# Kernel optimization log

Measured on AMD Instinct MI355X. Metric: run time of the kernel, lower is better.

Reference implementation:

```python
import jax, jax.numpy as jnp
import numpy as np

BS, SEQ, H = 64, 512, 768
E, T, K = 32, 64, 64


def setup_inputs() -> dict:
    key = jax.random.key(0)
    ks = jax.random.split(key, 16)
    return {
        "hidden_states": jax.random.normal(ks[0], (BS, SEQ, H), dtype=jnp.float32),
        "Wsrc": jax.random.normal(ks[1], (862, 384), dtype=jnp.float32) * 0.02,
        "Wtgt": jax.random.normal(ks[2], (862, 384), dtype=jnp.float32) * 0.02,
        "W_cls": jax.random.normal(ks[3], (2, 6144), dtype=jnp.float32) * 0.02,
        "b_cls": jnp.zeros((2,), dtype=jnp.float32),
        "W_topic": jax.random.normal(ks[4], (2, 6144), dtype=jnp.float32) * 0.02,
        "b_topic": jnp.zeros((2,), dtype=jnp.float32),
        "W_token": jax.random.normal(ks[5], (2, 6144), dtype=jnp.float32) * 0.02,
        "b_token": jnp.zeros((2,), dtype=jnp.float32),
        "source_ids": jax.random.randint(ks[6], (BS,), 0, 862),
        "target_ids": jax.random.randint(ks[7], (BS,), 0, 862),
        "ent_inds": jax.random.randint(ks[8], (BS, E), 0, SEQ - 1),
        "ent_mask": jnp.ones((BS, E), dtype=jnp.float32),
        "topic_inds": jax.random.randint(ks[9], (BS, T), 0, SEQ),
        "topic_mask": jnp.ones((BS, T), dtype=jnp.float32),
        "token_inds": jax.random.randint(ks[10], (BS, K), 0, SEQ),
        "token_mask": jnp.ones((BS, K), dtype=jnp.float32),
    }


def reference(hidden_states, Wsrc, Wtgt, W_cls, b_cls, W_topic, b_topic,
              W_token, b_token, source_ids, target_ids, ent_inds, ent_mask,
              topic_inds, topic_mask, token_inds, token_mask):
    bs = hidden_states.shape[0]
    # domain embedding: concat(source_emb, target_emb) -> [bs, 768] -> [bs, 96, 8]
    domain = jnp.concatenate([Wsrc[source_ids], Wtgt[target_ids]], axis=1)
    d0 = domain.reshape(bs, 96, 8)

    def gather(inds, mask, offset=0):
        # ragged gather of hidden states at token positions, zero-padded slots masked
        h = jnp.take_along_axis(hidden_states, (inds + offset)[:, :, None], axis=1)
        return h * mask[:, :, None]  # [bs, L, 768]

    ent_h = gather(ent_inds, ent_mask, offset=1)
    topic_h = gather(topic_inds, topic_mask)
    token_h = gather(token_inds, token_mask)

    # CLS bilinear: outer product over the 8-dim factor, [bs,96,8,8] -> [bs,6144]
    cls_h = hidden_states[:, 0, :].reshape(bs, 96, 8)
    bl_cls = (d0[:, :, :, None] * cls_h[:, :, None, :]).reshape(bs, 6144)
    cls_logits = jax.nn.softmax(bl_cls @ W_cls.T + b_cls, axis=1)

    def bilin(h, W, b):
        h4 = h.reshape(bs, -1, 96, 8)  # [bs, L, 96, 8]
        bl = (d0[:, None, :, :, None] * h4[:, :, :, None, :]).reshape(bs, h4.shape[1], 6144)
        return bl @ W.T + b  # [bs, L, n_out]

    topic_logits = jax.nn.softmax(bilin(topic_h, W_topic, b_topic), axis=2)
    token_logits = bilin(token_h, W_token, b_token)
    return cls_logits, topic_logits, token_logits
```

## Files before the change

kernel.cpp:

```cpp
#include <hip/hip_runtime.h>

#define BSZ 64
#define SEQ 512
#define HD  768
#define TT  64
#define NROW 6
#define NTASK 129

__global__ __launch_bounds__(256) void compute_V_kernel(
    const float* __restrict__ Wsrc,
    const float* __restrict__ Wtgt,
    const float* __restrict__ W_cls,
    const float* __restrict__ W_topic,
    const float* __restrict__ W_token,
    const int*   __restrict__ source_ids,
    const int*   __restrict__ target_ids,
    float*       __restrict__ Vg)
{
    __shared__ __align__(16) float dom[HD];
    const int b   = blockIdx.x;
    const int tid = threadIdx.x;

    const int sid = source_ids[b];
    const int tgt = target_ids[b];
    for (int j = tid; j < HD; j += 256)
        dom[j] = (j < 384) ? Wsrc[sid * 384 + j] : Wtgt[tgt * 384 + (j - 384)];
    __syncthreads();

    for (int idx = tid; idx < NROW * HD; idx += 256) {
        const int r = idx / HD;
        const int d = idx - r * HD;
        const int w = r >> 1, o = r & 1;
        const float* Wp = (w == 0) ? W_cls : (w == 1) ? W_topic : W_token;
        const int m = d >> 3, c = d & 7;
        const float* wrow = Wp + o * 6144 + m * 64 + c;
        float acc = 0.f;
        #pragma unroll
        for (int a = 0; a < 8; ++a)
            acc = fmaf(dom[m * 8 + a], wrow[a * 8], acc);
        Vg[(size_t)b * (NROW * HD) + idx] = acc;
    }
}

__global__ __launch_bounds__(256) void task_kernel(
    const float* __restrict__ hidden,
    const float* __restrict__ Vg,
    const float* __restrict__ b_cls,
    const float* __restrict__ b_topic,
    const float* __restrict__ b_token,
    const int*   __restrict__ topic_inds,
    const float* __restrict__ topic_mask,
    const int*   __restrict__ token_inds,
    const float* __restrict__ token_mask,
    float*       __restrict__ out)
{
    const int wg   = blockIdx.x * 4 + (threadIdx.x >> 6);
    const int lane = threadIdx.x & 63;
    const int b    = wg / NTASK;
    const int t    = wg - b * NTASK;

    int w, pos, outoff;
    float mask;
    const float* bias;
    bool do_softmax;
    if (t == 0) {
        w = 0; pos = 0; mask = 1.f; bias = b_cls; do_softmax = true;
        outoff = b * 2;
    } else if (t <= TT) {
        const int l = t - 1;
        w = 1; pos = topic_inds[b * TT + l]; mask = topic_mask[b * TT + l];
        bias = b_topic; do_softmax = true;
        outoff = 128 + (b * TT + l) * 2;
    } else {
        const int l = t - 1 - TT;
        w = 2; pos = token_inds[b * TT + l]; mask = token_mask[b * TT + l];
        bias = b_token; do_softmax = false;
        outoff = 128 + BSZ * TT * 2 + (b * TT + l) * 2;
    }

    const float4* hrow = reinterpret_cast<const float4*>(
        hidden + ((size_t)b * SEQ + (size_t)pos) * HD);
    const float4* v0 = reinterpret_cast<const float4*>(
        Vg + ((size_t)b * NROW + w * 2 + 0) * HD);
    const float4* v1 = reinterpret_cast<const float4*>(
        Vg + ((size_t)b * NROW + w * 2 + 1) * HD);

    float a0 = 0.f, a1 = 0.f;
    #pragma unroll
    for (int k = 0; k < 3; ++k) {
        const float4 h4 = hrow[lane + k * 64];
        const float4 x0 = v0[lane + k * 64];
        const float4 x1 = v1[lane + k * 64];
        a0 = fmaf(h4.x, x0.x, a0); a1 = fmaf(h4.x, x1.x, a1);
        a0 = fmaf(h4.y, x0.y, a0); a1 = fmaf(h4.y, x1.y, a1);
        a0 = fmaf(h4.z, x0.z, a0); a1 = fmaf(h4.z, x1.z, a1);
        a0 = fmaf(h4.w, x0.w, a0); a1 = fmaf(h4.w, x1.w, a1);
    }
    #pragma unroll
    for (int off = 32; off > 0; off >>= 1) {
        a0 += __shfl_down(a0, off, 64);
        a1 += __shfl_down(a1, off, 64);
    }

    if (lane == 0) {
        const float l0 = fmaf(mask, a0, bias[0]);
        const float l1 = fmaf(mask, a1, bias[1]);
        if (do_softmax) {
            const float mx = fmaxf(l0, l1);
            const float e0 = __expf(l0 - mx);
            const float e1 = __expf(l1 - mx);
            const float inv = 1.f / (e0 + e1);
            out[outoff]     = e0 * inv;
            out[outoff + 1] = e1 * inv;
        } else {
            out[outoff]     = l0;
            out[outoff + 1] = l1;
        }
    }
}

extern "C" void kernel_launch(void* const* d_in, const int* in_sizes, int n_in,
                              void* d_out, int out_size, void* d_ws, size_t ws_size,
                              hipStream_t stream) {
    const float* hidden     = (const float*)d_in[0];
    const float* Wsrc       = (const float*)d_in[1];
    const float* Wtgt       = (const float*)d_in[2];
    const float* W_cls      = (const float*)d_in[3];
    const float* b_cls      = (const float*)d_in[4];
    const float* W_topic    = (const float*)d_in[5];
    const float* b_topic    = (const float*)d_in[6];
    const float* W_token    = (const float*)d_in[7];
    const float* b_token    = (const float*)d_in[8];
    const int*   source_ids = (const int*)d_in[9];
    const int*   target_ids = (const int*)d_in[10];
    const int*   topic_inds = (const int*)d_in[13];
    const float* topic_mask = (const float*)d_in[14];
    const int*   token_inds = (const int*)d_in[15];
    const float* token_mask = (const float*)d_in[16];
    float* out = (float*)d_out;
    float* Vg  = (float*)d_ws;

    compute_V_kernel<<<BSZ, 256, 0, stream>>>(
        Wsrc, Wtgt, W_cls, W_topic, W_token, source_ids, target_ids, Vg);

    task_kernel<<<(BSZ * NTASK) / 4, 256, 0, stream>>>(
        hidden, Vg, b_cls, b_topic, b_token,
        topic_inds, topic_mask, token_inds, token_mask, out);
}
```

Measured before the change: 165.7 us.

## Fuse V computation and task dot products into one kernel using shared memory

Merges the two kernels into one. Each of four blocks per batch recomputes the 6x768 V matrix into LDS and then handles about 32 of the 129 tasks, two tasks per wave per iteration. This drops a kernel launch and the global round trip for V, and the paired tasks give more memory parallelism per wave. In exchange, V is computed four times per batch, and only 256 blocks are launched where there were about 2064 before, which may limit how much latency can be hidden.

```diff
diff --git a/kernel.cpp b/kernel.cpp
--- a/kernel.cpp
+++ b/kernel.cpp
@@ -6,19 +6,31 @@
 #define TT  64
 #define NROW 6
 #define NTASK 129
+#define QPB  4
 
-__global__ __launch_bounds__(256) void compute_V_kernel(
+__global__ __launch_bounds__(256) void fused_kernel(
+    const float* __restrict__ hidden,
     const float* __restrict__ Wsrc,
     const float* __restrict__ Wtgt,
     const float* __restrict__ W_cls,
+    const float* __restrict__ b_cls,
     const float* __restrict__ W_topic,
+    const float* __restrict__ b_topic,
     const float* __restrict__ W_token,
+    const float* __restrict__ b_token,
     const int*   __restrict__ source_ids,
     const int*   __restrict__ target_ids,
-    float*       __restrict__ Vg)
+    const int*   __restrict__ topic_inds,
+    const float* __restrict__ topic_mask,
+    const int*   __restrict__ token_inds,
+    const float* __restrict__ token_mask,
+    float*       __restrict__ out)
 {
     __shared__ __align__(16) float dom[HD];
-    const int b   = blockIdx.x;
+    __shared__ __align__(16) float V[NROW * HD];
+
+    const int b   = blockIdx.x >> 2;
+    const int q   = blockIdx.x & 3;
     const int tid = threadIdx.x;
 
     const int sid = source_ids[b];
@@ -38,83 +50,122 @@
         #pragma unroll
         for (int a = 0; a < 8; ++a)
             acc = fmaf(dom[m * 8 + a], wrow[a * 8], acc);
-        Vg[(size_t)b * (NROW * HD) + idx] = acc;
+        V[idx] = acc;
     }
-}
+    __syncthreads();
 
-__global__ __launch_bounds__(256) void task_kernel(
-    const float* __restrict__ hidden,
-    const float* __restrict__ Vg,
-    const float* __restrict__ b_cls,
-    const float* __restrict__ b_topic,
-    const float* __restrict__ b_token,
-    const int*   __restrict__ topic_inds,
-    const float* __restrict__ topic_mask,
-    const int*   __restrict__ token_inds,
-    const float* __restrict__ token_mask,
-    float*       __restrict__ out)
-{
-    const int wg   = blockIdx.x * 4 + (threadIdx.x >> 6);
-    const int lane = threadIdx.x & 63;
-    const int b    = wg / NTASK;
-    const int t    = wg - b * NTASK;
+    const int wave = tid >> 6;
+    const int lane = tid & 63;
+    const int tbase = (q == 0) ? 0 : 33 + 32 * (q - 1);
+    const int tend  = (q == 0) ? 33 : tbase + 32;
 
-    int w, pos, outoff;
-    float mask;
-    const float* bias;
-    bool do_softmax;
-    if (t == 0) {
-        w = 0; pos = 0; mask = 1.f; bias = b_cls; do_softmax = true;
-        outoff = b * 2;
-    } else if (t <= TT) {
-        const int l = t - 1;
-        w = 1; pos = topic_inds[b * TT + l]; mask = topic_mask[b * TT + l];
-        bias = b_topic; do_softmax = true;
-        outoff = 128 + (b * TT + l) * 2;
-    } else {
-        const int l = t - 1 - TT;
-        w = 2; pos = token_inds[b * TT + l]; mask = token_mask[b * TT + l];
-        bias = b_token; do_softmax = false;
-        outoff = 128 + BSZ * TT * 2 + (b * TT + l) * 2;
-    }
+    const float bc0 = b_cls[0],   bc1 = b_cls[1];
+    const float bp0 = b_topic[0], bp1 = b_topic[1];
+    const float bk0 = b_token[0], bk1 = b_token[1];
 
-    const float4* hrow = reinterpret_cast<const float4*>(
-        hidden + ((size_t)b * SEQ + (size_t)pos) * HD);
-    const float4* v0 = reinterpret_cast<const float4*>(
-        Vg + ((size_t)b * NROW + w * 2 + 0) * HD);
-    const float4* v1 = reinterpret_cast<const float4*>(
-        Vg + ((size_t)b * NROW + w * 2 + 1) * HD);
+    for (int tA = tbase + wave; tA < tend; tA += 8) {
+        const int tB = tA + 4;
+        const bool hasB = (tB < tend);
 
-    float a0 = 0.f, a1 = 0.f;
-    #pragma unroll
-    for (int k = 0; k < 3; ++k) {
-        const float4 h4 = hrow[lane + k * 64];
-        const float4 x0 = v0[lane + k * 64];
-        const float4 x1 = v1[lane + k * 64];
-        a0 = fmaf(h4.x, x0.x, a0); a1 = fmaf(h4.x, x1.x, a1);
-        a0 = fmaf(h4.y, x0.y, a0); a1 = fmaf(h4.y, x1.y, a1);
-        a0 = fmaf(h4.z, x0.z, a0); a1 = fmaf(h4.z, x1.z, a1);
-        a0 = fmaf(h4.w, x0.w, a0); a1 = fmaf(h4.w, x1.w, a1);
-    }
-    #pragma unroll
-    for (int off = 32; off > 0; off >>= 1) {
-        a0 += __shfl_down(a0, off, 64);
-        a1 += __shfl_down(a1, off, 64);
-    }
+        int wA, posA, offA; float mA; bool smA;
+        int wB = 0, posB = 0, offB = 0; float mB = 0.f; bool smB = false;
+        {
+            const int t = tA;
+            if (t == 0) { wA = 0; posA = 0; mA = 1.f; smA = true; offA = b * 2; }
+            else if (t <= TT) {
+                const int l = t - 1;
+                wA = 1; posA = topic_inds[b * TT + l]; mA = topic_mask[b * TT + l];
+                smA = true; offA = 128 + (b * TT + l) * 2;
+            } else {
+                const int l = t - 1 - TT;
+                wA = 2; posA = token_inds[b * TT + l]; mA = token_mask[b * TT + l];
+                smA = false; offA = 128 + BSZ * TT * 2 + (b * TT + l) * 2;
+            }
+        }
+        if (hasB) {
+            const int t = tB;
+            if (t <= TT) {
+                const int l = t - 1;
+                wB = 1; posB = topic_inds[b * TT + l]; mB = topic_mask[b * TT + l];
+                smB = true; offB = 128 + (b * TT + l) * 2;
+            } else {
+                const int l = t - 1 - TT;
+                wB = 2; posB = token_inds[b * TT + l]; mB = token_mask[b * TT + l];
+                smB = false; offB = 128 + BSZ * TT * 2 + (b * TT + l) * 2;
+            }
+        }
 
-    if (lane == 0) {
-        const float l0 = fmaf(mask, a0, bias[0]);
-        const float l1 = fmaf(mask, a1, bias[1]);
-        if (do_softmax) {
-            const float mx = fmaxf(l0, l1);
-            const float e0 = __expf(l0 - mx);
-            const float e1 = __expf(l1 - mx);
-            const float inv = 1.f / (e0 + e1);
-            out[outoff]     = e0 * inv;
-            out[outoff + 1] = e1 * inv;
-        } else {
-            out[outoff]     = l0;
-            out[outoff + 1] = l1;
+        const float4* hA = reinterpret_cast<const float4*>(
+            hidden + ((size_t)b * SEQ + (size_t)posA) * HD);
+        const float4* hB = reinterpret_cast<const float4*>(
+            hidden + ((size_t)b * SEQ + (size_t)posB) * HD);
+        float4 ra0 = hA[lane], ra1 = hA[lane + 64], ra2 = hA[lane + 128];
+        float4 rb0, rb1, rb2;
+        if (hasB) { rb0 = hB[lane]; rb1 = hB[lane + 64]; rb2 = hB[lane + 128]; }
+
+        const float4* vA0 = reinterpret_cast<const float4*>(&V[(wA * 2 + 0) * HD]);
+        const float4* vA1 = reinterpret_cast<const float4*>(&V[(wA * 2 + 1) * HD]);
+        const float4* vB0 = reinterpret_cast<const float4*>(&V[(wB * 2 + 0) * HD]);
+        const float4* vB1 = reinterpret_cast<const float4*>(&V[(wB * 2 + 1) * HD]);
+
+        float a0 = 0.f, a1 = 0.f, c0 = 0.f, c1 = 0.f;
+        #define DOT(h4, x0, x1, A0, A1)                          \
+            { A0 = fmaf(h4.x, x0.x, A0); A1 = fmaf(h4.x, x1.x, A1); \
+              A0 = fmaf(h4.y, x0.y, A0); A1 = fmaf(h4.y, x1.y, A1); \
+              A0 = fmaf(h4.z, x0.z, A0); A1 = fmaf(h4.z, x1.z, A1); \
+              A0 = fmaf(h4.w, x0.w, A0); A1 = fmaf(h4.w, x1.w, A1); }
+        {
+            float4 x0, x1;
+            x0 = vA0[lane];       x1 = vA1[lane];       DOT(ra0, x0, x1, a0, a1);
+            x0 = vA0[lane + 64];  x1 = vA1[lane + 64];  DOT(ra1, x0, x1, a0, a1);
+            x0 = vA0[lane + 128]; x1 = vA1[lane + 128]; DOT(ra2, x0, x1, a0, a1);
+            if (hasB) {
+                x0 = vB0[lane];       x1 = vB1[lane];       DOT(rb0, x0, x1, c0, c1);
+                x0 = vB0[lane + 64];  x1 = vB1[lane + 64];  DOT(rb1, x0, x1, c0, c1);
+                x0 = vB0[lane + 128]; x1 = vB1[lane + 128]; DOT(rb2, x0, x1, c0, c1);
+            }
+        }
+        #undef DOT
+
+        #pragma unroll
+        for (int off = 32; off > 0; off >>= 1) {
+            a0 += __shfl_down(a0, off, 64);
+            a1 += __shfl_down(a1, off, 64);
+            c0 += __shfl_down(c0, off, 64);
+            c1 += __shfl_down(c1, off, 64);
+        }
+
+        if (lane == 0) {
+            {
+                const float bb0 = (wA == 0) ? bc0 : (wA == 1) ? bp0 : bk0;
+                const float bb1 = (wA == 0) ? bc1 : (wA == 1) ? bp1 : bk1;
+                const float l0 = fmaf(mA, a0, bb0);
+                const float l1 = fmaf(mA, a1, bb1);
+                if (smA) {
+                    const float mx = fmaxf(l0, l1);
+                    const float e0 = __expf(l0 - mx);
+                    const float e1 = __expf(l1 - mx);
+                    const float inv = 1.f / (e0 + e1);
+                    out[offA] = e0 * inv; out[offA + 1] = e1 * inv;
+                } else {
+                    out[offA] = l0; out[offA + 1] = l1;
+                }
+            }
+            if (hasB) {
+                const float bb0 = (wB == 1) ? bp0 : bk0;
+                const float bb1 = (wB == 1) ? bp1 : bk1;
+                const float l0 = fmaf(mB, c0, bb0);
+                const float l1 = fmaf(mB, c1, bb1);
+                if (smB) {
+                    const float mx = fmaxf(l0, l1);
+                    const float e0 = __expf(l0 - mx);
+                    const float e1 = __expf(l1 - mx);
+                    const float inv = 1.f / (e0 + e1);
+                    out[offB] = e0 * inv; out[offB + 1] = e1 * inv;
+                } else {
+                    out[offB] = l0; out[offB + 1] = l1;
+                }
+            }
         }
     }
 }
@@ -138,12 +189,8 @@
     const int*   token_inds = (const int*)d_in[15];
     const float* token_mask = (const float*)d_in[16];
     float* out = (float*)d_out;
-    float* Vg  = (float*)d_ws;
 
-    compute_V_kernel<<<BSZ, 256, 0, stream>>>(
-        Wsrc, Wtgt, W_cls, W_topic, W_token, source_ids, target_ids, Vg);
-
-    task_kernel<<<(BSZ * NTASK) / 4, 256, 0, stream>>>(
-        hidden, Vg, b_cls, b_topic, b_token,
-        topic_inds, topic_mask, token_inds, token_mask, out);
+    fused_kernel<<<BSZ * QPB, 256, 0, stream>>>(
+        hidden, Wsrc, Wtgt, W_cls, b_cls, W_topic, b_topic, W_token, b_token,
+        source_ids, target_ids, topic_inds, topic_mask, token_inds, token_mask, out);
 }
```

Result: no change. 166.1 us (+0.3%).
